# Kernel optimization log

Measured on AMD Instinct MI355X. Metric: run time of the kernel, lower is better.

## Reference

```python
import jax, jax.numpy as jnp
import numpy as np

L, B, N, D, H, DH, MLP = 4, 4, 2048, 512, 8, 64, 2048
EPS = 1e-5


def layer_norm(x, w, b):
    mu = jnp.mean(x, axis=-1, keepdims=True)
    var = jnp.mean(jnp.square(x - mu), axis=-1, keepdims=True)
    return (x - mu) * jax.lax.rsqrt(var + EPS) * w + b


def setup_inputs() -> dict:
    key = jax.random.key(0)
    ks = jax.random.split(key, 8)
    x = jax.random.normal(ks[0], (B, N, D), dtype=jnp.float32)
    # mask == 1.0 means blocked: triu(ones) - eye -> strict upper triangle
    mask = jnp.triu(jnp.ones((N, N), dtype=jnp.float32)) - jnp.eye(N, dtype=jnp.float32)
    s = 0.02
    return {
        "x": x,
        "mask": mask,
        "ln1_w": jnp.ones((L, D), jnp.float32),
        "ln1_b": jnp.zeros((L, D), jnp.float32),
        "w_qkv": jax.random.normal(ks[1], (L, D, 3 * H * DH), jnp.float32) * s,
        "w_out": jax.random.normal(ks[2], (L, H * DH, D), jnp.float32) * s,
        "b_out": jnp.zeros((L, D), jnp.float32),
        "ln2_w": jnp.ones((L, D), jnp.float32),
        "ln2_b": jnp.zeros((L, D), jnp.float32),
        "w1": jax.random.normal(ks[3], (L, D, MLP), jnp.float32) * s,
        "b1": jnp.zeros((L, MLP), jnp.float32),
        "w2": jax.random.normal(ks[4], (L, MLP, D), jnp.float32) * s,
        "b2": jnp.zeros((L, D), jnp.float32),
    }


def reference(x, mask, ln1_w, ln1_b, w_qkv, w_out, b_out, ln2_w, ln2_b, w1, b1, w2, b2):
    scale = DH ** (-0.5)
    blocked = (mask == 1.0)  # [N, N]
    for l in range(L):
        # --- masked self-attention (pre-norm) ---
        h = layer_norm(x, ln1_w[l], ln1_b[l])
        qkv = h @ w_qkv[l]                               # [B, N, 3*H*DH]
        q, k, v = jnp.split(qkv, 3, axis=-1)
        q = q.reshape(B, N, H, DH).transpose(0, 2, 1, 3)  # bhnd
        k = k.reshape(B, N, H, DH).transpose(0, 2, 1, 3)
        v = v.reshape(B, N, H, DH).transpose(0, 2, 1, 3)
        scores = jnp.einsum('bhnd,bhmd->bhnm', q, k) * scale
        scores = jnp.where(blocked, -jnp.inf, scores)
        att = jax.nn.softmax(scores, axis=-1)
        o = jnp.einsum('bhnm,bhmd->bhnd', att, v)
        o = o.transpose(0, 2, 1, 3).reshape(B, N, H * DH)
        x = x + (o @ w_out[l] + b_out[l])
        # --- GELU MLP (pre-norm) ---
        h2 = layer_norm(x, ln2_w[l], ln2_b[l])
        ff = jax.nn.gelu(h2 @ w1[l] + b1[l], approximate=False) @ w2[l] + b2[l]
        x = x + ff
    return x
```

## Files before the change

kernel.cpp:

```cpp
#include <hip/hip_runtime.h>
#include <math.h>

#define L 4
#define BATCH 4
#define N 2048
#define D 512
#define H 8
#define DH 64
#define MLPD 2048
#define M_ROWS (BATCH * N)
#define VTP 2064

using v8s = __attribute__((ext_vector_type(8))) short;
using v4f = __attribute__((ext_vector_type(4))) float;

__device__ inline short f2bf(float f) {
  union { float f; unsigned u; } v; v.f = f;
  unsigned r = v.u + 0x7FFFu + ((v.u >> 16) & 1u);
  return (short)(r >> 16);
}
__device__ inline unsigned pack2bf_t(float a, float b) {
  union { float f; unsigned u; } x, y; x.f = a; y.f = b;
  return (x.u >> 16) | (y.u & 0xFFFF0000u);
}

#define MFMA(a, b, c) __builtin_amdgcn_mfma_f32_16x16x32_bf16(a, b, c, 0, 0, 0)

__device__ __forceinline__ void gload_lds16(const void* g, void* l) {
  __builtin_amdgcn_global_load_lds((const __attribute__((address_space(1))) void*)g,
                                   (__attribute__((address_space(3))) void*)l, 16, 0, 0);
}

#define FENCE asm volatile("" ::: "memory")
#define BAR  do { FENCE; __builtin_amdgcn_s_barrier(); FENCE; } while (0)
#define VMW(n) asm volatile("s_waitcnt vmcnt(" #n ")" ::: "memory")

__global__ void copyf4_kernel(const float4* __restrict__ in, float4* __restrict__ out, int n) {
  int i = blockIdx.x * blockDim.x + threadIdx.x;
  if (i < n) out[i] = in[i];
}

__launch_bounds__(256)
__global__ void transpose_w_kernel(const float* __restrict__ src, short* __restrict__ dst,
                                   int R, int C, int qcols) {
  __shared__ float tile[32][33];
  const size_t base = (size_t)blockIdx.z * R * C;
  const int c0 = blockIdx.x * 32, r0 = blockIdx.y * 32;
  const int tx = threadIdx.x & 31, ty = threadIdx.x >> 5;
  #pragma unroll
  for (int i = ty; i < 32; i += 8)
    tile[i][tx] = src[base + (size_t)(r0 + i) * C + c0 + tx];
  __syncthreads();
  #pragma unroll
  for (int i = ty; i < 32; i += 8) {
    float val = tile[tx][i];
    if (c0 + i < qcols) val *= 0.125f;
    dst[base + (size_t)(c0 + i) * R + r0 + tx] = f2bf(val);
  }
}

__launch_bounds__(256)
__global__ void ln_kernel(const float* __restrict__ x, const float* __restrict__ w,
                          const float* __restrict__ b, short* __restrict__ out) {
  const int row = blockIdx.x * 4 + (threadIdx.x >> 6);
  const int lane = threadIdx.x & 63;
  const float* xr = x + (size_t)row * D;
  float4 a0 = *(const float4*)(xr + lane * 8);
  float4 a1 = *(const float4*)(xr + lane * 8 + 4);
  float v[8] = {a0.x, a0.y, a0.z, a0.w, a1.x, a1.y, a1.z, a1.w};
  float s = 0.f;
  #pragma unroll
  for (int j = 0; j < 8; ++j) s += v[j];
  #pragma unroll
  for (int m = 1; m < 64; m <<= 1) s += __shfl_xor(s, m, 64);
  const float mean = s * (1.0f / D);
  float q = 0.f;
  #pragma unroll
  for (int j = 0; j < 8; ++j) { float d = v[j] - mean; q += d * d; }
  #pragma unroll
  for (int m = 1; m < 64; m <<= 1) q += __shfl_xor(q, m, 64);
  const float rstd = rsqrtf(q * (1.0f / D) + 1e-5f);
  float4 w0 = *(const float4*)(w + lane * 8);
  float4 w1 = *(const float4*)(w + lane * 8 + 4);
  float4 b0 = *(const float4*)(b + lane * 8);
  float4 b1 = *(const float4*)(b + lane * 8 + 4);
  float wv[8] = {w0.x, w0.y, w0.z, w0.w, w1.x, w1.y, w1.z, w1.w};
  float bv[8] = {b0.x, b0.y, b0.z, b0.w, b1.x, b1.y, b1.z, b1.w};
  v8s r;
  #pragma unroll
  for (int j = 0; j < 8; ++j) r[j] = f2bf((v[j] - mean) * rstd * wv[j] + bv[j]);
  *(v8s*)(out + (size_t)row * D + lane * 8) = r;
}

template <int MODE, int NT>
__launch_bounds__(512, 2)
__global__ void gemm256_kernel(const short* __restrict__ A, const short* __restrict__ Bt,
                               const float* __restrict__ bias, void* __restrict__ Out,
                               short* __restrict__ Vt, int M, int Nc) {
  constexpr int K = NT * 64;
  __shared__ __align__(16) short Ah[4][128 * 64];
  __shared__ __align__(16) short Bh[4][128 * 64];
  const int tid = threadIdx.x, lane = tid & 63, w = tid >> 6;
  const int wr = w >> 2, wc = w & 3;
  const int r16 = lane & 15, g = lane >> 4;

  const int nxb = Nc >> 8;
  const int nyb = M >> 8;
  const int bid = (int)blockIdx.x;
  const int xcd = bid & 7, ii = bid >> 3;
  const int byi = xcd * (nyb >> 3) + ii / nxb;
  const int bxi = ii % nxb;
  const int m0 = byi << 8, n0 = bxi << 8;

  const int srow = lane >> 3;
  const int ssw = ((lane & 7) ^ srow) * 8;

  const short* Abase = A + (size_t)(m0 + srow) * K + ssw;
  const short* Bbase = Bt + (size_t)(n0 + srow) * K + ssw;

  auto STAGE_A = [&](int j) {
    const int jc = (j > 2 * NT - 1) ? (2 * NT - 1) : j;
    const int slot = j & 3, k0 = (jc >> 1) * 64, r0 = (jc & 1) * 128;
    #pragma unroll
    for (int i = 0; i < 2; ++i) {
      const int rr = i * 64 + w * 8;
      gload_lds16(Abase + (size_t)(r0 + rr) * K + k0, (char*)&Ah[slot][0] + rr * 128);
    }
  };
  auto STAGE_B = [&](int j) {
    const int jc = (j > 2 * NT - 1) ? (2 * NT - 1) : j;
    const int slot = j & 3, k0 = (jc >> 1) * 64, c0 = (jc & 1) * 128;
    #pragma unroll
    for (int i = 0; i < 2; ++i) {
      const int rr = i * 64 + w * 8;
      gload_lds16(Bbase + (size_t)(c0 + rr) * K + k0, (char*)&Bh[slot][0] + rr * 128);
    }
  };

  const int arow = wr * 64 + r16;
  const int brow = wc * 32 + r16;
  const int swz7 = r16 & 7;

  v8s ar[4][2], br0[2][2], br1[2][2];
  auto LDA = [&](int slot) {
    const char* base = (const char*)&Ah[slot][0];
    #pragma unroll
    for (int mf = 0; mf < 4; ++mf)
      #pragma unroll
      for (int kh = 0; kh < 2; ++kh)
        ar[mf][kh] = *(const v8s*)(base + (arow + mf * 16) * 128 + (((kh * 4 + g) ^ swz7) * 16));
  };
  auto LDB0 = [&](int slot) {
    const char* base = (const char*)&Bh[slot][0];
    #pragma unroll
    for (int nf = 0; nf < 2; ++nf)
      #pragma unroll
      for (int kh = 0; kh < 2; ++kh)
        br0[nf][kh] = *(const v8s*)(base + (brow + nf * 16) * 128 + (((kh * 4 + g) ^ swz7) * 16));
  };
  auto LDB1 = [&](int slot) {
    const char* base = (const char*)&Bh[slot][0];
    #pragma unroll
    for (int nf = 0; nf < 2; ++nf)
      #pragma unroll
      for (int kh = 0; kh < 2; ++kh)
        br1[nf][kh] = *(const v8s*)(base + (brow + nf * 16) * 128 + (((kh * 4 + g) ^ swz7) * 16));
  };

  v4f acc[2][2][4][2] = {};

#define MMA_Q(QM, QN, BR)                                                      \
  do {                                                                         \
    __builtin_amdgcn_s_setprio(1);                                             \
    _Pragma("unroll")                                                          \
    for (int kh = 0; kh < 2; ++kh)                                             \
      _Pragma("unroll")                                                        \
      for (int mf = 0; mf < 4; ++mf)                                           \
        _Pragma("unroll")                                                      \
        for (int nf = 0; nf < 2; ++nf)                                         \
          acc[QM][QN][mf][nf] = MFMA(ar[mf][kh], BR[nf][kh], acc[QM][QN][mf][nf]); \
    __builtin_amdgcn_s_setprio(0);                                             \
  } while (0)

  STAGE_A(0); STAGE_B(0); STAGE_B(1); STAGE_A(1); STAGE_A(2); STAGE_B(2); STAGE_B(3);
  VMW(6);
  BAR;

  auto KTILE = [&](int T, int sa) {
    LDA(sa); LDB0(sa);
    STAGE_A(2 * T + 3);
    BAR;
    MMA_Q(0, 0, br0);
    BAR;
    LDB1(sa + 1);
    BAR;
    MMA_Q(0, 1, br1);
    BAR;
    LDA(sa + 1);
    STAGE_A(2 * T + 4); STAGE_B(2 * T + 4);
    BAR;
    MMA_Q(1, 1, br1);
    BAR;
    STAGE_B(2 * T + 5);
    BAR;
    MMA_Q(1, 0, br0);
    VMW(6);
    BAR;
  };

  #pragma unroll
  for (int t2 = 0; t2 < NT / 2; ++t2) {
    KTILE(2 * t2, 0);
    KTILE(2 * t2 + 1, 2);
  }
#undef MMA_Q

  if constexpr (MODE == 3) {
    if (n0 >= 1024) {
      const int bb = m0 >> 11;
      const int cperm = 16 * (g >> 1) + 8 * (g & 1);
      #pragma unroll
      for (int qm = 0; qm < 2; ++qm)
        #pragma unroll
        for (int mf = 0; mf < 4; ++mf) {
          const int key0 = m0 + qm * 128 + wr * 64 + mf * 16;
          const int ng = (key0 & 2047) & ~63;
          const int c = ((key0 & 63) & 32) + cperm + 32 * (mf >> 1) % 32;
          const int ccol = 32 * (mf >> 1) + cperm + 4 * (mf & 1);
          (void)c;
          #pragma unroll
          for (int qn = 0; qn < 2; ++qn)
            #pragma unroll
            for (int nf = 0; nf < 2; ++nf) {
              const int col = n0 + qn * 128 + wc * 32 + nf * 16 + r16;
              const int dhg = col - 1024;
              const int bh = bb * 8 + (dhg >> 6);
              short* dst = Vt + (size_t)(bh * 64 + (dhg & 63)) * VTP + ng + ccol;
              uint2 st;
              st.x = (unsigned)(unsigned short)f2bf(acc[qm][qn][mf][nf][0]) |
                     ((unsigned)(unsigned short)f2bf(acc[qm][qn][mf][nf][1]) << 16);
              st.y = (unsigned)(unsigned short)f2bf(acc[qm][qn][mf][nf][2]) |
                     ((unsigned)(unsigned short)f2bf(acc[qm][qn][mf][nf][3]) << 16);
              *(uint2*)dst = st;
            }
        }
      return;
    }
  }
  #pragma unroll
  for (int qm = 0; qm < 2; ++qm)
    #pragma unroll
    for (int mf = 0; mf < 4; ++mf) {
      const int row = m0 + qm * 128 + wr * 64 + mf * 16 + g * 4;
      #pragma unroll
      for (int qn = 0; qn < 2; ++qn)
        #pragma unroll
        for (int nf = 0; nf < 2; ++nf) {
          const int col = n0 + qn * 128 + wc * 32 + nf * 16 + r16;
          float bv = 0.0f;
          if constexpr (MODE == 1) bv = bias[col];
          #pragma unroll
          for (int r = 0; r < 4; ++r) {
            float val = acc[qm][qn][mf][nf][r] + bv;
            if constexpr (MODE == 1) {
              const float z = val * 0.70710678118f;
              const float az = fabsf(z);
              const float t = 1.0f / (1.0f + 0.3275911f * az);
              const float p =
                  0.254829592f +
                  t * (-0.284496736f + t * (1.421413741f + t * (-1.453152027f + t * 1.061405429f)));
              float er = 1.0f - p * t * __expf(-az * az);
              er = (z < 0.0f) ? -er : er;
              val = 0.5f * val * (1.0f + er);
            }
            ((short*)Out)[(size_t)(row + r) * Nc + col] = f2bf(val);
          }
        }
    }
}

template <int MODE, int BN>
__launch_bounds__(256)
__global__ void gemm128_kernel(const short* __restrict__ A, const short* __restrict__ Bt,
                               const float* __restrict__ bias, const float* __restrict__ Xres,
                               void* __restrict__ Out, int M, int Nc, int K) {
  constexpr int MR = (BN == 128) ? 4 : 2;
  __shared__ __align__(16) short As[2][128 * 64];
  __shared__ __align__(16) short Bs[2][BN * 64];
  const int tid = threadIdx.x;
  const int lane = tid & 63;
  const int w = tid >> 6;
  const int wr = (BN == 128) ? (w >> 1) : w;
  const int wc = (BN == 128) ? (w & 1) : 0;
  const int r16 = lane & 15, g = lane >> 4;

  const int nxb = Nc / BN;
  const int nyb = M >> 7;
  const int bid = (int)blockIdx.x;
  const int xcd = bid & 7;
  const int ii = bid >> 3;
  const int byi = xcd * (nyb >> 3) + ii / nxb;
  const int bxi = ii % nxb;
  const int m0 = byi * 128, n0 = bxi * BN;

  const int srow = lane >> 3;
  const int ssw = ((lane & 7) ^ srow) * 8;

  auto STAGE = [&](int buf, int k0) {
    #pragma unroll
    for (int j = 0; j < 4; ++j) {
      const int row = w * 32 + j * 8;
      gload_lds16(A + (size_t)(m0 + row + srow) * K + k0 + ssw,
                  (char*)&As[buf][0] + row * 128);
    }
    #pragma unroll
    for (int j = 0; j < BN / 32; ++j) {
      const int row = w * (BN / 4) + j * 8;
      gload_lds16(Bt + (size_t)(n0 + row + srow) * K + k0 + ssw,
                  (char*)&Bs[buf][0] + row * 128);
    }
  };

  v4f acc[MR][4] = {};

  STAGE(0, 0);
  __syncthreads();
  int cur = 0;
  for (int k0 = 0; k0 < K; k0 += 64) {
    if (k0 + 64 < K) STAGE(cur ^ 1, k0 + 64);
    v8s af[MR][2], bf[4][2];
    #pragma unroll
    for (int m = 0; m < MR; ++m) {
      const int row = wr * (MR * 16) + m * 16 + r16;
      #pragma unroll
      for (int kh = 0; kh < 2; ++kh)
        af[m][kh] = *(const v8s*)((const char*)&As[cur][0] + row * 128 +
                                  (((kh * 4 + g) ^ (row & 7)) * 16));
    }
    #pragma unroll
    for (int n = 0; n < 4; ++n) {
      const int row = wc * 64 + n * 16 + r16;
      #pragma unroll
      for (int kh = 0; kh < 2; ++kh)
        bf[n][kh] = *(const v8s*)((const char*)&Bs[cur][0] + row * 128 +
                                  (((kh * 4 + g) ^ (row & 7)) * 16));
    }
    #pragma unroll
    for (int kh = 0; kh < 2; ++kh)
      #pragma unroll
      for (int m = 0; m < MR; ++m)
        #pragma unroll
        for (int n = 0; n < 4; ++n)
          acc[m][n] = MFMA(af[m][kh], bf[n][kh], acc[m][n]);
    __syncthreads();
    cur ^= 1;
  }

  #pragma unroll
  for (int m = 0; m < MR; ++m) {
    const int row = m0 + wr * (MR * 16) + m * 16 + g * 4;
    #pragma unroll
    for (int n = 0; n < 4; ++n) {
      const int col = n0 + wc * 64 + n * 16 + r16;
      const float bv = bias ? bias[col] : 0.0f;
      #pragma unroll
      for (int r = 0; r < 4; ++r) {
        const size_t idx = (size_t)(row + r) * Nc + col;
        float val = acc[m][n][r] + bv;
        if constexpr (MODE == 0) {
          ((short*)Out)[idx] = f2bf(val);
        } else if constexpr (MODE == 1) {
          const float z = val * 0.70710678118f;
          const float az = fabsf(z);
          const float t = 1.0f / (1.0f + 0.3275911f * az);
          const float p =
              0.254829592f +
              t * (-0.284496736f + t * (1.421413741f + t * (-1.453152027f + t * 1.061405429f)));
          float er = 1.0f - p * t * __expf(-az * az);
          er = (z < 0.0f) ? -er : er;
          val = 0.5f * val * (1.0f + er);
          ((short*)Out)[idx] = f2bf(val);
        } else {
          ((float*)Out)[idx] = val + Xres[idx];
        }
      }
    }
  }
}

__launch_bounds__(256)
__global__ void attn_kernel(const short* __restrict__ qkv, const short* __restrict__ Vt,
                            short* __restrict__ o) {
  __shared__ __align__(16) short Ks[3][64 * 64];
  __shared__ __align__(16) short Vs[2][64 * 64];
  const int lin = (int)blockIdx.x;
  const int bh = ((lin >> 3) & 3) * 8 + (lin & 7);
  const int xl2 = 31 - (lin >> 5);
  const int b = bh >> 3, h = bh & 7;
  const int q0 = xl2 * 64;
  const int tid = threadIdx.x, lane = tid & 63, w = tid >> 6;
  const int r16 = lane & 15, g = lane >> 4;
  const int qw = q0 + w * 16;

  v8s qf0, qf1;
  {
    const size_t qbase = ((size_t)(b * N + qw + r16)) * 1536 + h * 64;
    qf0 = *(const v8s*)(qkv + qbase + g * 8);
    qf1 = *(const v8s*)(qkv + qbase + 32 + g * 8);
  }

  const short* vtb = Vt + (size_t)bh * 64 * VTP;

  const int srow = lane >> 3;
  const int ssw = ((lane & 7) ^ srow) * 8;

  v4f oacc[4] = {};
  float lsum = 0.f;
  const int tdiag = xl2;

  auto STAGE_K = [&](int t) {
    t = (t > tdiag) ? tdiag : t;
    const int k0 = t * 64, buf = t % 3;
    #pragma unroll
    for (int j = 0; j < 2; ++j) {
      const int row = w * 16 + j * 8;
      gload_lds16(qkv + ((size_t)(b * N + k0 + row + srow)) * 1536 + 512 + h * 64 + ssw,
                  (char*)&Ks[buf][0] + row * 128);
    }
  };
  auto STAGE_V = [&](int t) {
    t = (t > tdiag) ? tdiag : t;
    const int k0 = t * 64, buf = t & 1;
    #pragma unroll
    for (int j = 0; j < 2; ++j) {
      const int row = w * 16 + j * 8;
      gload_lds16(vtb + (size_t)(row + srow) * VTP + k0 + ssw,
                  (char*)&Vs[buf][0] + row * 128);
    }
  };

  STAGE_K(0); STAGE_V(0); STAGE_K(1);

  for (int t = 0; t <= tdiag; ++t) {
    VMW(2);
    BAR;
    STAGE_V(t + 1);
    STAGE_K(t + 2);

    const char* kb = (const char*)&Ks[t % 3][0];
    const char* vb = (const char*)&Vs[t & 1][0];

    v8s vf[4][2];
    #pragma unroll
    for (int a = 0; a < 4; ++a)
      #pragma unroll
      for (int c = 0; c < 2; ++c)
        vf[a][c] = *(const v8s*)(vb + (a * 16 + r16) * 128 + (((c * 4 + g) ^ (r16 & 7)) * 16));

    __builtin_amdgcn_s_setprio(1);
    v4f s[4];
    #pragma unroll
    for (int kt = 0; kt < 4; ++kt) {
      const int krow = (kt * 16 + r16) * 128;
      v8s kfa = *(const v8s*)(kb + krow + ((g ^ (r16 & 7)) * 16));
      v8s kfb = *(const v8s*)(kb + krow + (((4 + g) ^ (r16 & 7)) * 16));
      v4f ss = {};
      ss = MFMA(kfa, qf0, ss);
      ss = MFMA(kfb, qf1, ss);
      s[kt] = ss;
    }
    __builtin_amdgcn_s_setprio(0);

    const bool needmask = (t == tdiag);
    const int qrow = qw + r16;
    const int kbase = t * 64 + 4 * g;
    unsigned pw_[8];
    #pragma unroll
    for (int kt = 0; kt < 4; ++kt) {
      float e[4];
      #pragma unroll
      for (int r = 0; r < 4; ++r) {
        float v = s[kt][r];
        if (needmask && (kbase + kt * 16 + r > qrow)) v = -3e38f;
        e[r] = __expf(v);
      }
      lsum += (e[0] + e[1]) + (e[2] + e[3]);
      pw_[kt * 2 + 0] = pack2bf_t(e[0], e[1]);
      pw_[kt * 2 + 1] = pack2bf_t(e[2], e[3]);
    }
    union PU { unsigned u[4]; v8s s8; };
    PU pa0, pa1;
    pa0.u[0] = pw_[0]; pa0.u[1] = pw_[1]; pa0.u[2] = pw_[2]; pa0.u[3] = pw_[3];
    pa1.u[0] = pw_[4]; pa1.u[1] = pw_[5]; pa1.u[2] = pw_[6]; pa1.u[3] = pw_[7];

    __builtin_amdgcn_s_setprio(1);
    #pragma unroll
    for (int dt = 0; dt < 4; ++dt) oacc[dt] = MFMA(pa0.s8, vf[dt][0], oacc[dt]);
    #pragma unroll
    for (int dt = 0; dt < 4; ++dt) oacc[dt] = MFMA(pa1.s8, vf[dt][1], oacc[dt]);
    __builtin_amdgcn_s_setprio(0);
  }

  lsum += __shfl_xor(lsum, 16, 64);
  lsum += __shfl_xor(lsum, 32, 64);
  const float linv = 1.0f / lsum;
  float ldiv[4];
  #pragma unroll
  for (int r = 0; r < 4; ++r) ldiv[r] = __shfl(linv, g * 4 + r, 64);

  #pragma unroll
  for (int dt = 0; dt < 4; ++dt)
    #pragma unroll
    for (int r = 0; r < 4; ++r) {
      const float val = oacc[dt][r] * ldiv[r];
      o[((size_t)(b * N + qw + g * 4 + r)) * 512 + h * 64 + dt * 16 + r16] = f2bf(val);
    }
}

extern "C" void kernel_launch(void* const* d_in, const int* in_sizes, int n_in,
                              void* d_out, int out_size, void* d_ws, size_t ws_size,
                              hipStream_t stream) {
  const float* x_in  = (const float*)d_in[0];
  const float* ln1_w = (const float*)d_in[2];
  const float* ln1_b = (const float*)d_in[3];
  const float* w_qkv = (const float*)d_in[4];
  const float* w_out = (const float*)d_in[5];
  const float* b_out = (const float*)d_in[6];
  const float* ln2_w = (const float*)d_in[7];
  const float* ln2_b = (const float*)d_in[8];
  const float* w1    = (const float*)d_in[9];
  const float* b1    = (const float*)d_in[10];
  const float* w2    = (const float*)d_in[11];
  const float* b2    = (const float*)d_in[12];

  char* ws = (char*)d_ws;
  size_t off = 0;
  auto alloc = [&](size_t bytes) { char* p = ws + off; off += (bytes + 255) & ~(size_t)255; return p; };
  short* wqkvT = (short*)alloc((size_t)L * 1536 * 512 * 2);
  short* woutT = (short*)alloc((size_t)L * 512 * 512 * 2);
  short* w1T   = (short*)alloc((size_t)L * 512 * 2048 * 2);
  short* w2T   = (short*)alloc((size_t)L * 2048 * 512 * 2);
  short* hln   = (short*)alloc((size_t)M_ROWS * 512 * 2);
  short* big   = (short*)alloc((size_t)M_ROWS * 2048 * 2);
  short* oatt  = (short*)alloc((size_t)M_ROWS * 512 * 2);
  short* Vtg   = (short*)alloc((size_t)BATCH * H * 64 * VTP * 2);
  short* qkv = big;
  short* ff  = big;

  float* x = (float*)d_out;

  copyf4_kernel<<<4096, 256, 0, stream>>>((const float4*)x_in, (float4*)x, M_ROWS * D / 4);

  transpose_w_kernel<<<dim3(1536 / 32, 512 / 32, L), 256, 0, stream>>>(w_qkv, wqkvT, 512, 1536, 512);
  transpose_w_kernel<<<dim3(512 / 32, 512 / 32, L), 256, 0, stream>>>(w_out, woutT, 512, 512, 0);
  transpose_w_kernel<<<dim3(2048 / 32, 512 / 32, L), 256, 0, stream>>>(w1, w1T, 512, 2048, 0);
  transpose_w_kernel<<<dim3(512 / 32, 2048 / 32, L), 256, 0, stream>>>(w2, w2T, 2048, 512, 0);

  for (int l = 0; l < L; ++l) {
    ln_kernel<<<M_ROWS / 4, 256, 0, stream>>>(x, ln1_w + l * 512, ln1_b + l * 512, hln);
    gemm256_kernel<3, 8><<<dim3((1536 / 256) * (M_ROWS / 256)), 512, 0, stream>>>(
        hln, wqkvT + (size_t)l * 1536 * 512, nullptr, qkv, Vtg, M_ROWS, 1536);
    attn_kernel<<<dim3(1024), 256, 0, stream>>>(qkv, Vtg, oatt);
    gemm128_kernel<2, 64><<<dim3((512 / 64) * (M_ROWS / 128)), 256, 0, stream>>>(
        oatt, woutT + (size_t)l * 512 * 512, b_out + l * 512, x, x, M_ROWS, 512, 512);
    ln_kernel<<<M_ROWS / 4, 256, 0, stream>>>(x, ln2_w + l * 512, ln2_b + l * 512, hln);
    gemm256_kernel<1, 8><<<dim3((2048 / 256) * (M_ROWS / 256)), 512, 0, stream>>>(
        hln, w1T + (size_t)l * 512 * 2048, b1 + l * 2048, ff, nullptr, M_ROWS, 2048);
    gemm128_kernel<2, 64><<<dim3((512 / 64) * (M_ROWS / 128)), 256, 0, stream>>>(
        ff, w2T + (size_t)l * 2048 * 512, b2 + l * 512, x, x, M_ROWS, 512, 2048);
  }
}
```

Measured before the change: 604.7 us.

## Software-pipeline PV MFMA one tile behind QK and softmax in attention

```diff
diff --git a/kernel.cpp b/kernel.cpp
--- a/kernel.cpp
+++ b/kernel.cpp
@@ -225,9 +225,7 @@
         for (int mf = 0; mf < 4; ++mf) {
           const int key0 = m0 + qm * 128 + wr * 64 + mf * 16;
           const int ng = (key0 & 2047) & ~63;
-          const int c = ((key0 & 63) & 32) + cperm + 32 * (mf >> 1) % 32;
           const int ccol = 32 * (mf >> 1) + cperm + 4 * (mf & 1);
-          (void)c;
           #pragma unroll
           for (int qn = 0; qn < 2; ++qn)
             #pragma unroll
@@ -439,6 +437,10 @@
     }
   };
 
+  union PU { unsigned u[4]; v8s s8; };
+  v8s vfp[4][2];
+  unsigned ppk[8];
+
   STAGE_K(0); STAGE_V(0); STAGE_K(1);
 
   for (int t = 0; t <= tdiag; ++t) {
@@ -447,15 +449,26 @@
     STAGE_V(t + 1);
     STAGE_K(t + 2);
 
+    if (t > 0) {
+      PU pa0, pa1;
+      pa0.u[0] = ppk[0]; pa0.u[1] = ppk[1]; pa0.u[2] = ppk[2]; pa0.u[3] = ppk[3];
+      pa1.u[0] = ppk[4]; pa1.u[1] = ppk[5]; pa1.u[2] = ppk[6]; pa1.u[3] = ppk[7];
+      __builtin_amdgcn_s_setprio(1);
+      #pragma unroll
+      for (int dt = 0; dt < 4; ++dt) oacc[dt] = MFMA(pa0.s8, vfp[dt][0], oacc[dt]);
+      #pragma unroll
+      for (int dt = 0; dt < 4; ++dt) oacc[dt] = MFMA(pa1.s8, vfp[dt][1], oacc[dt]);
+      __builtin_amdgcn_s_setprio(0);
+    }
+
     const char* kb = (const char*)&Ks[t % 3][0];
     const char* vb = (const char*)&Vs[t & 1][0];
 
-    v8s vf[4][2];
     #pragma unroll
     for (int a = 0; a < 4; ++a)
       #pragma unroll
       for (int c = 0; c < 2; ++c)
-        vf[a][c] = *(const v8s*)(vb + (a * 16 + r16) * 128 + (((c * 4 + g) ^ (r16 & 7)) * 16));
+        vfp[a][c] = *(const v8s*)(vb + (a * 16 + r16) * 128 + (((c * 4 + g) ^ (r16 & 7)) * 16));
 
     __builtin_amdgcn_s_setprio(1);
     v4f s[4];
@@ -474,7 +487,6 @@
     const bool needmask = (t == tdiag);
     const int qrow = qw + r16;
     const int kbase = t * 64 + 4 * g;
-    unsigned pw_[8];
     #pragma unroll
     for (int kt = 0; kt < 4; ++kt) {
       float e[4];
@@ -485,20 +497,19 @@
         e[r] = __expf(v);
       }
       lsum += (e[0] + e[1]) + (e[2] + e[3]);
-      pw_[kt * 2 + 0] = pack2bf_t(e[0], e[1]);
-      pw_[kt * 2 + 1] = pack2bf_t(e[2], e[3]);
-    }
-    union PU { unsigned u[4]; v8s s8; };
+      ppk[kt * 2 + 0] = pack2bf_t(e[0], e[1]);
+      ppk[kt * 2 + 1] = pack2bf_t(e[2], e[3]);
+    }
+  }
+
+  {
     PU pa0, pa1;
-    pa0.u[0] = pw_[0]; pa0.u[1] = pw_[1]; pa0.u[2] = pw_[2]; pa0.u[3] = pw_[3];
-    pa1.u[0] = pw_[4]; pa1.u[1] = pw_[5]; pa1.u[2] = pw_[6]; pa1.u[3] = pw_[7];
-
-    __builtin_amdgcn_s_setprio(1);
-    #pragma unroll
-    for (int dt = 0; dt < 4; ++dt) oacc[dt] = MFMA(pa0.s8, vf[dt][0], oacc[dt]);
-    #pragma unroll
-    for (int dt = 0; dt < 4; ++dt) oacc[dt] = MFMA(pa1.s8, vf[dt][1], oacc[dt]);
-    __builtin_amdgcn_s_setprio(0);
+    pa0.u[0] = ppk[0]; pa0.u[1] = ppk[1]; pa0.u[2] = ppk[2]; pa0.u[3] = ppk[3];
+    pa1.u[0] = ppk[4]; pa1.u[1] = ppk[5]; pa1.u[2] = ppk[6]; pa1.u[3] = ppk[7];
+    #pragma unroll
+    for (int dt = 0; dt < 4; ++dt) oacc[dt] = MFMA(pa0.s8, vfp[dt][0], oacc[dt]);
+    #pragma unroll
+    for (int dt = 0; dt < 4; ++dt) oacc[dt] = MFMA(pa1.s8, vfp[dt][1], oacc[dt]);
   }
 
   lsum += __shfl_xor(lsum, 16, 64);
```

Result: slower. 620.6 us (+2.6%).

## Double attention query tile per block to reuse K/V tiles across 128 query rows

Applied to the files above, without the earlier changes.

```diff
diff --git a/kernel.cpp b/kernel.cpp
--- a/kernel.cpp
+++ b/kernel.cpp
@@ -225,9 +225,7 @@
         for (int mf = 0; mf < 4; ++mf) {
           const int key0 = m0 + qm * 128 + wr * 64 + mf * 16;
           const int ng = (key0 & 2047) & ~63;
-          const int c = ((key0 & 63) & 32) + cperm + 32 * (mf >> 1) % 32;
           const int ccol = 32 * (mf >> 1) + cperm + 4 * (mf & 1);
-          (void)c;
           #pragma unroll
           for (int qn = 0; qn < 2; ++qn)
             #pragma unroll
@@ -394,19 +392,24 @@
   __shared__ __align__(16) short Ks[3][64 * 64];
   __shared__ __align__(16) short Vs[2][64 * 64];
   const int lin = (int)blockIdx.x;
-  const int bh = ((lin >> 3) & 3) * 8 + (lin & 7);
-  const int xl2 = 31 - (lin >> 5);
+  const int xcd = lin & 7;
+  const int kk = lin >> 3;
+  const int bh = (kk & 3) * 8 + xcd;
+  const int xl = (kk < 32) ? (15 - (kk >> 2)) : ((kk - 32) >> 2);
   const int b = bh >> 3, h = bh & 7;
-  const int q0 = xl2 * 64;
+  const int q0 = xl * 128;
   const int tid = threadIdx.x, lane = tid & 63, w = tid >> 6;
   const int r16 = lane & 15, g = lane >> 4;
-  const int qw = q0 + w * 16;
-
-  v8s qf0, qf1;
+  const int qw = q0 + w * 32;
+
+  v8s qa0, qa1, qb0, qb1;
   {
-    const size_t qbase = ((size_t)(b * N + qw + r16)) * 1536 + h * 64;
-    qf0 = *(const v8s*)(qkv + qbase + g * 8);
-    qf1 = *(const v8s*)(qkv + qbase + 32 + g * 8);
+    const size_t qA = ((size_t)(b * N + qw + r16)) * 1536 + h * 64;
+    const size_t qB = ((size_t)(b * N + qw + 16 + r16)) * 1536 + h * 64;
+    qa0 = *(const v8s*)(qkv + qA + g * 8);
+    qa1 = *(const v8s*)(qkv + qA + 32 + g * 8);
+    qb0 = *(const v8s*)(qkv + qB + g * 8);
+    qb1 = *(const v8s*)(qkv + qB + 32 + g * 8);
   }
 
   const short* vtb = Vt + (size_t)bh * 64 * VTP;
@@ -414,9 +417,11 @@
   const int srow = lane >> 3;
   const int ssw = ((lane & 7) ^ srow) * 8;
 
-  v4f oacc[4] = {};
-  float lsum = 0.f;
-  const int tdiag = xl2;
+  v4f oaccA[4] = {}, oaccB[4] = {};
+  float lsumA = 0.f, lsumB = 0.f;
+  const int tdiag = 2 * xl + 1;
+  const int wlast = 2 * xl + (w >> 1);
+  const int nt = 2 * xl + 2;
 
   auto STAGE_K = [&](int t) {
     t = (t > tdiag) ? tdiag : t;
@@ -441,79 +446,110 @@
 
   STAGE_K(0); STAGE_V(0); STAGE_K(1);
 
-  for (int t = 0; t <= tdiag; ++t) {
+  for (int t = 0; t < nt; ++t) {
     VMW(2);
     BAR;
     STAGE_V(t + 1);
     STAGE_K(t + 2);
 
-    const char* kb = (const char*)&Ks[t % 3][0];
-    const char* vb = (const char*)&Vs[t & 1][0];
-
-    v8s vf[4][2];
-    #pragma unroll
-    for (int a = 0; a < 4; ++a)
-      #pragma unroll
-      for (int c = 0; c < 2; ++c)
-        vf[a][c] = *(const v8s*)(vb + (a * 16 + r16) * 128 + (((c * 4 + g) ^ (r16 & 7)) * 16));
-
-    __builtin_amdgcn_s_setprio(1);
-    v4f s[4];
-    #pragma unroll
-    for (int kt = 0; kt < 4; ++kt) {
-      const int krow = (kt * 16 + r16) * 128;
-      v8s kfa = *(const v8s*)(kb + krow + ((g ^ (r16 & 7)) * 16));
-      v8s kfb = *(const v8s*)(kb + krow + (((4 + g) ^ (r16 & 7)) * 16));
-      v4f ss = {};
-      ss = MFMA(kfa, qf0, ss);
-      ss = MFMA(kfb, qf1, ss);
-      s[kt] = ss;
-    }
-    __builtin_amdgcn_s_setprio(0);
-
-    const bool needmask = (t == tdiag);
-    const int qrow = qw + r16;
-    const int kbase = t * 64 + 4 * g;
-    unsigned pw_[8];
-    #pragma unroll
-    for (int kt = 0; kt < 4; ++kt) {
-      float e[4];
-      #pragma unroll
-      for (int r = 0; r < 4; ++r) {
-        float v = s[kt][r];
-        if (needmask && (kbase + kt * 16 + r > qrow)) v = -3e38f;
-        e[r] = __expf(v);
+    if (t <= wlast) {
+      const char* kb = (const char*)&Ks[t % 3][0];
+      const char* vb = (const char*)&Vs[t & 1][0];
+
+      v8s vf[4][2];
+      #pragma unroll
+      for (int a = 0; a < 4; ++a)
+        #pragma unroll
+        for (int c = 0; c < 2; ++c)
+          vf[a][c] = *(const v8s*)(vb + (a * 16 + r16) * 128 + (((c * 4 + g) ^ (r16 & 7)) * 16));
+
+      __builtin_amdgcn_s_setprio(1);
+      v4f sA[4], sB[4];
+      #pragma unroll
+      for (int kt = 0; kt < 4; ++kt) {
+        const int krow = (kt * 16 + r16) * 128;
+        v8s kfa = *(const v8s*)(kb + krow + ((g ^ (r16 & 7)) * 16));
+        v8s kfb = *(const v8s*)(kb + krow + (((4 + g) ^ (r16 & 7)) * 16));
+        v4f ss = {};
+        ss = MFMA(kfa, qa0, ss);
+        ss = MFMA(kfb, qa1, ss);
+        sA[kt] = ss;
+        v4f tt = {};
+        tt = MFMA(kfa, qb0, tt);
+        tt = MFMA(kfb, qb1, tt);
+        sB[kt] = tt;
       }
-      lsum += (e[0] + e[1]) + (e[2] + e[3]);
-      pw_[kt * 2 + 0] = pack2bf_t(e[0], e[1]);
-      pw_[kt * 2 + 1] = pack2bf_t(e[2], e[3]);
-    }
-    union PU { unsigned u[4]; v8s s8; };
-    PU pa0, pa1;
-    pa0.u[0] = pw_[0]; pa0.u[1] = pw_[1]; pa0.u[2] = pw_[2]; pa0.u[3] = pw_[3];
-    pa1.u[0] = pw_[4]; pa1.u[1] = pw_[5]; pa1.u[2] = pw_[6]; pa1.u[3] = pw_[7];
-
-    __builtin_amdgcn_s_setprio(1);
-    #pragma unroll
-    for (int dt = 0; dt < 4; ++dt) oacc[dt] = MFMA(pa0.s8, vf[dt][0], oacc[dt]);
-    #pragma unroll
-    for (int dt = 0; dt < 4; ++dt) oacc[dt] = MFMA(pa1.s8, vf[dt][1], oacc[dt]);
-    __builtin_amdgcn_s_setprio(0);
-  }
-
-  lsum += __shfl_xor(lsum, 16, 64);
-  lsum += __shfl_xor(lsum, 32, 64);
-  const float linv = 1.0f / lsum;
-  float ldiv[4];
-  #pragma unroll
-  for (int r = 0; r < 4; ++r) ldiv[r] = __shfl(linv, g * 4 + r, 64);
+      __builtin_amdgcn_s_setprio(0);
+
+      const bool needmask = (t == wlast);
+      const int qrowA = qw + r16;
+      const int qrowB = qw + 16 + r16;
+      const int kbase = t * 64 + 4 * g;
+      unsigned pwA[8], pwB[8];
+      #pragma unroll
+      for (int kt = 0; kt < 4; ++kt) {
+        float eA[4], eB[4];
+        #pragma unroll
+        for (int r = 0; r < 4; ++r) {
+          const int key = kbase + kt * 16 + r;
+          float va = sA[kt][r], vb2 = sB[kt][r];
+          if (needmask) {
+            if (key > qrowA) va = -3e38f;
+            if (key > qrowB) vb2 = -3e38f;
+          }
+          eA[r] = __expf(va);
+          eB[r] = __expf(vb2);
+        }
+        lsumA += (eA[0] + eA[1]) + (eA[2] + eA[3]);
+        lsumB += (eB[0] + eB[1]) + (eB[2] + eB[3]);
+        pwA[kt * 2 + 0] = pack2bf_t(eA[0], eA[1]);
+        pwA[kt * 2 + 1] = pack2bf_t(eA[2], eA[3]);
+        pwB[kt * 2 + 0] = pack2bf_t(eB[0], eB[1]);
+        pwB[kt * 2 + 1] = pack2bf_t(eB[2], eB[3]);
+      }
+      union PU { unsigned u[4]; v8s s8; };
+      PU pA0, pA1, pB0, pB1;
+      pA0.u[0] = pwA[0]; pA0.u[1] = pwA[1]; pA0.u[2] = pwA[2]; pA0.u[3] = pwA[3];
+      pA1.u[0] = pwA[4]; pA1.u[1] = pwA[5]; pA1.u[2] = pwA[6]; pA1.u[3] = pwA[7];
+      pB0.u[0] = pwB[0]; pB0.u[1] = pwB[1]; pB0.u[2] = pwB[2]; pB0.u[3] = pwB[3];
+      pB1.u[0] = pwB[4]; pB1.u[1] = pwB[5]; pB1.u[2] = pwB[6]; pB1.u[3] = pwB[7];
+
+      __builtin_amdgcn_s_setprio(1);
+      #pragma unroll
+      for (int dt = 0; dt < 4; ++dt) {
+        oaccA[dt] = MFMA(pA0.s8, vf[dt][0], oaccA[dt]);
+        oaccB[dt] = MFMA(pB0.s8, vf[dt][0], oaccB[dt]);
+      }
+      #pragma unroll
+      for (int dt = 0; dt < 4; ++dt) {
+        oaccA[dt] = MFMA(pA1.s8, vf[dt][1], oaccA[dt]);
+        oaccB[dt] = MFMA(pB1.s8, vf[dt][1], oaccB[dt]);
+      }
+      __builtin_amdgcn_s_setprio(0);
+    }
+  }
+
+  lsumA += __shfl_xor(lsumA, 16, 64);
+  lsumA += __shfl_xor(lsumA, 32, 64);
+  lsumB += __shfl_xor(lsumB, 16, 64);
+  lsumB += __shfl_xor(lsumB, 32, 64);
+  const float linvA = 1.0f / lsumA;
+  const float linvB = 1.0f / lsumB;
+  float ldA[4], ldB[4];
+  #pragma unroll
+  for (int r = 0; r < 4; ++r) {
+    ldA[r] = __shfl(linvA, g * 4 + r, 64);
+    ldB[r] = __shfl(linvB, g * 4 + r, 64);
+  }
 
   #pragma unroll
   for (int dt = 0; dt < 4; ++dt)
     #pragma unroll
     for (int r = 0; r < 4; ++r) {
-      const float val = oacc[dt][r] * ldiv[r];
-      o[((size_t)(b * N + qw + g * 4 + r)) * 512 + h * 64 + dt * 16 + r16] = f2bf(val);
+      o[((size_t)(b * N + qw + g * 4 + r)) * 512 + h * 64 + dt * 16 + r16] =
+          f2bf(oaccA[dt][r] * ldA[r]);
+      o[((size_t)(b * N + qw + 16 + g * 4 + r)) * 512 + h * 64 + dt * 16 + r16] =
+          f2bf(oaccB[dt][r] * ldB[r]);
     }
 }
 
@@ -560,7 +596,7 @@
     ln_kernel<<<M_ROWS / 4, 256, 0, stream>>>(x, ln1_w + l * 512, ln1_b + l * 512, hln);
     gemm256_kernel<3, 8><<<dim3((1536 / 256) * (M_ROWS / 256)), 512, 0, stream>>>(
         hln, wqkvT + (size_t)l * 1536 * 512, nullptr, qkv, Vtg, M_ROWS, 1536);
-    attn_kernel<<<dim3(1024), 256, 0, stream>>>(qkv, Vtg, oatt);
+    attn_kernel<<<dim3(512), 256, 0, stream>>>(qkv, Vtg, oatt);
     gemm128_kernel<2, 64><<<dim3((512 / 64) * (M_ROWS / 128)), 256, 0, stream>>>(
         oatt, woutT + (size_t)l * 512 * 512, b_out + l * 512, x, x, M_ROWS, 512, 512);
     ln_kernel<<<M_ROWS / 4, 256, 0, stream>>>(x, ln2_w + l * 512, ln2_b + l * 512, hln);
```

New measurement: 666.6 us. 1.1x slower.

## Drop input copy kernel and load V fragments directly from global

Applied to the files above, without the earlier changes.

```diff
diff --git a/kernel.cpp b/kernel.cpp
--- a/kernel.cpp
+++ b/kernel.cpp
@@ -34,11 +34,6 @@
 #define FENCE asm volatile("" ::: "memory")
 #define BAR  do { FENCE; __builtin_amdgcn_s_barrier(); FENCE; } while (0)
 #define VMW(n) asm volatile("s_waitcnt vmcnt(" #n ")" ::: "memory")
-
-__global__ void copyf4_kernel(const float4* __restrict__ in, float4* __restrict__ out, int n) {
-  int i = blockIdx.x * blockDim.x + threadIdx.x;
-  if (i < n) out[i] = in[i];
-}
 
 __launch_bounds__(256)
 __global__ void transpose_w_kernel(const float* __restrict__ src, short* __restrict__ dst,
@@ -225,9 +220,7 @@
         for (int mf = 0; mf < 4; ++mf) {
           const int key0 = m0 + qm * 128 + wr * 64 + mf * 16;
           const int ng = (key0 & 2047) & ~63;
-          const int c = ((key0 & 63) & 32) + cperm + 32 * (mf >> 1) % 32;
           const int ccol = 32 * (mf >> 1) + cperm + 4 * (mf & 1);
-          (void)c;
           #pragma unroll
           for (int qn = 0; qn < 2; ++qn)
             #pragma unroll
@@ -392,7 +385,6 @@
 __global__ void attn_kernel(const short* __restrict__ qkv, const short* __restrict__ Vt,
                             short* __restrict__ o) {
   __shared__ __align__(16) short Ks[3][64 * 64];
-  __shared__ __align__(16) short Vs[2][64 * 64];
   const int lin = (int)blockIdx.x;
   const int bh = ((lin >> 3) & 3) * 8 + (lin & 7);
   const int xl2 = 31 - (lin >> 5);
@@ -410,6 +402,7 @@
   }
 
   const short* vtb = Vt + (size_t)bh * 64 * VTP;
+  const short* vrow = vtb + (size_t)r16 * VTP;
 
   const int srow = lane >> 3;
   const int ssw = ((lane & 7) ^ srow) * 8;
@@ -428,34 +421,24 @@
                   (char*)&Ks[buf][0] + row * 128);
     }
   };
-  auto STAGE_V = [&](int t) {
-    t = (t > tdiag) ? tdiag : t;
-    const int k0 = t * 64, buf = t & 1;
-    #pragma unroll
-    for (int j = 0; j < 2; ++j) {
-      const int row = w * 16 + j * 8;
-      gload_lds16(vtb + (size_t)(row + srow) * VTP + k0 + ssw,
-                  (char*)&Vs[buf][0] + row * 128);
-    }
-  };
-
-  STAGE_K(0); STAGE_V(0); STAGE_K(1);
+
+  STAGE_K(0); STAGE_K(1);
 
   for (int t = 0; t <= tdiag; ++t) {
     VMW(2);
     BAR;
-    STAGE_V(t + 1);
+
+    const int k0 = t * 64;
+    v8s vf[4][2];
+    #pragma unroll
+    for (int a = 0; a < 4; ++a)
+      #pragma unroll
+      for (int c = 0; c < 2; ++c)
+        vf[a][c] = *(const v8s*)(vrow + (size_t)(a * 16) * VTP + k0 + c * 32 + g * 8);
+
     STAGE_K(t + 2);
 
     const char* kb = (const char*)&Ks[t % 3][0];
-    const char* vb = (const char*)&Vs[t & 1][0];
-
-    v8s vf[4][2];
-    #pragma unroll
-    for (int a = 0; a < 4; ++a)
-      #pragma unroll
-      for (int c = 0; c < 2; ++c)
-        vf[a][c] = *(const v8s*)(vb + (a * 16 + r16) * 128 + (((c * 4 + g) ^ (r16 & 7)) * 16));
 
     __builtin_amdgcn_s_setprio(1);
     v4f s[4];
@@ -549,20 +532,19 @@
 
   float* x = (float*)d_out;
 
-  copyf4_kernel<<<4096, 256, 0, stream>>>((const float4*)x_in, (float4*)x, M_ROWS * D / 4);
-
   transpose_w_kernel<<<dim3(1536 / 32, 512 / 32, L), 256, 0, stream>>>(w_qkv, wqkvT, 512, 1536, 512);
   transpose_w_kernel<<<dim3(512 / 32, 512 / 32, L), 256, 0, stream>>>(w_out, woutT, 512, 512, 0);
   transpose_w_kernel<<<dim3(2048 / 32, 512 / 32, L), 256, 0, stream>>>(w1, w1T, 512, 2048, 0);
   transpose_w_kernel<<<dim3(512 / 32, 2048 / 32, L), 256, 0, stream>>>(w2, w2T, 2048, 512, 0);
 
   for (int l = 0; l < L; ++l) {
-    ln_kernel<<<M_ROWS / 4, 256, 0, stream>>>(x, ln1_w + l * 512, ln1_b + l * 512, hln);
+    const float* xl = (l == 0) ? x_in : x;
+    ln_kernel<<<M_ROWS / 4, 256, 0, stream>>>(xl, ln1_w + l * 512, ln1_b + l * 512, hln);
     gemm256_kernel<3, 8><<<dim3((1536 / 256) * (M_ROWS / 256)), 512, 0, stream>>>(
         hln, wqkvT + (size_t)l * 1536 * 512, nullptr, qkv, Vtg, M_ROWS, 1536);
     attn_kernel<<<dim3(1024), 256, 0, stream>>>(qkv, Vtg, oatt);
     gemm128_kernel<2, 64><<<dim3((512 / 64) * (M_ROWS / 128)), 256, 0, stream>>>(
-        oatt, woutT + (size_t)l * 512 * 512, b_out + l * 512, x, x, M_ROWS, 512, 512);
+        oatt, woutT + (size_t)l * 512 * 512, b_out + l * 512, xl, x, M_ROWS, 512, 512);
     ln_kernel<<<M_ROWS / 4, 256, 0, stream>>>(x, ln2_w + l * 512, ln2_b + l * 512, hln);
     gemm256_kernel<1, 8><<<dim3((2048 / 256) * (M_ROWS / 256)), 512, 0, stream>>>(
         hln, w1T + (size_t)l * 512 * 2048, b1 + l * 2048, ff, nullptr, M_ROWS, 2048);
```

New measurement: 694.2 us. 14.8% more time.
